# Optimization experiments

Measured on AMD Instinct MI355X. Metric: run time of the kernel, lower is better.

## Reference

```python
import jax, jax.numpy as jnp
import numpy as np

N = 100_000   # nodes
E = 1_600_000 # edges (avg degree 16)
D = 128       # dim == dim_out
NEG_SLOPE = 0.2  # PyG GATConv default


def setup_inputs() -> dict:
    key = jax.random.key(0)
    ks = jax.random.split(key, 11)
    s = 1.0 / np.sqrt(D)
    return {
        "x": jax.random.normal(ks[0], (N, D), jnp.float32),
        "edge_index": jax.random.randint(ks[1], (2, E), 0, N, jnp.int32),
        "W1": jax.random.normal(ks[2], (D, D), jnp.float32) * s,
        "a_src1": jax.random.normal(ks[3], (D,), jnp.float32) * s,
        "a_dst1": jax.random.normal(ks[4], (D,), jnp.float32) * s,
        "b1": jnp.zeros((D,), jnp.float32),
        "W2": jax.random.normal(ks[5], (D, D), jnp.float32) * s,
        "a_src2": jax.random.normal(ks[6], (D,), jnp.float32) * s,
        "a_dst2": jax.random.normal(ks[7], (D,), jnp.float32) * s,
        "b2": jnp.zeros((D,), jnp.float32),
    }


def gat_conv(x, W, a_src, a_dst, b, src, dst, n):
    # PyG GATConv, heads=1: message flows src (j) -> dst (i)
    h = x @ W                              # [n, d]
    al_src = h @ a_src                     # per-node src attention logit
    al_dst = h @ a_dst                     # per-node dst attention logit
    e = jax.nn.leaky_relu(al_src[src] + al_dst[dst], NEG_SLOPE)  # [E']
    # softmax over incoming edges of each destination node (segment softmax)
    m = jax.ops.segment_max(e, dst, num_segments=n)
    e = jnp.exp(e - m[dst])
    z = jax.ops.segment_sum(e, dst, num_segments=n)
    alpha = e / z[dst]                     # [E']
    out = jax.ops.segment_sum(h[src] * alpha[:, None], dst, num_segments=n)
    return out + b


def reference(x, edge_index, W1, a_src1, a_dst1, b1, W2, a_src2, a_dst2, b2):
    n = x.shape[0]
    loop = jnp.arange(n, dtype=edge_index.dtype)
    src = jnp.concatenate([edge_index[0], loop])  # add_self_loops=True
    dst = jnp.concatenate([edge_index[1], loop])
    h = gat_conv(x, W1, a_src1, a_dst1, b1, src, dst, n)
    # self_loops=True -> residual=False; dropout in eval mode = identity
    return gat_conv(h, W2, a_src2, a_dst2, b2, src, dst, n)
```

## Files before the change

### kernel.cpp

```cpp
#include <hip/hip_runtime.h>
#include <hip/hip_bf16.h>
#include <math.h>

#define D 128
#define LRELU_SLOPE 0.2f
#define BSH 9
#define BSZ 512
#define BCAP 10240
#define SC_CHUNK 2048

typedef __attribute__((ext_vector_type(8))) short bf16x8;
typedef __attribute__((ext_vector_type(4))) float f32x4;

__device__ __forceinline__ float lrelu(float x){ return x > 0.f ? x : LRELU_SLOPE * x; }

__device__ __forceinline__ unsigned short bf16_rn(float x){
  unsigned int u = __float_as_uint(x);
  return (unsigned short)((u + 0x7FFFu + ((u >> 16) & 1u)) >> 16);
}
__device__ __forceinline__ float bf16_lo_f(unsigned int u){ return __uint_as_float(u << 16); }
__device__ __forceinline__ float bf16_hi_f(unsigned int u){ return __uint_as_float(u & 0xFFFF0000u); }

__device__ __forceinline__ unsigned int enc_f(float f){
  unsigned int u = __float_as_uint(f);
  return (u & 0x80000000u) ? ~u : (u | 0x80000000u);
}
__device__ __forceinline__ float dec_f(unsigned int e){
  return __uint_as_float((e & 0x80000000u) ? (e & 0x7FFFFFFFu) : ~e);
}

__device__ __forceinline__ int colmap(int p){ return ((p & 7) << 4) + (p >> 3); }

__global__ __launch_bounds__(256) void prep_kernel(const float* __restrict__ W1,
    const float* __restrict__ W2,
    const float* __restrict__ as1, const float* __restrict__ ad1,
    const float* __restrict__ as2, const float* __restrict__ ad2,
    const float* __restrict__ b1,
    unsigned short* __restrict__ Whf1, unsigned short* __restrict__ Wlf1,
    unsigned short* __restrict__ Whf2, unsigned short* __restrict__ Wlf2,
    unsigned short* __restrict__ Whfx1, unsigned short* __restrict__ Wlfx1,
    unsigned short* __restrict__ Whfx2, unsigned short* __restrict__ Wlfx2,
    float* __restrict__ bias_perm1,
    unsigned int* __restrict__ mx, int* __restrict__ bcur, int nbuck)
{
  __shared__ float wa[2][128];
  int blk = blockIdx.x;
  if (blk < 128){
    bool layer2 = (blk >= 64);
    const float* W = layer2 ? W2 : W1;
    unsigned short* Whf = layer2 ? Whf2 : Whf1;
    unsigned short* Wlf = layer2 ? Wlf2 : Wlf1;
    int t = (blk & 63)*256 + threadIdx.x;
    int k  = t >> 7;
    int nn = t & 127;
    float w = W[t];
    unsigned short h = bf16_rn(w);
    float whf = __uint_as_float(((unsigned int)h) << 16);
    unsigned short l = bf16_rn(w - whf);
    int ks = layer2 ? (((k & 15) << 3) + (k >> 4)) : k;
    int kc = ks >> 5, l4 = (ks >> 3) & 3, e = ks & 7;
    int cf = nn >> 4, l15 = nn & 15;
    int idx = ((kc*8 + cf)*64 + l4*16 + l15)*8 + e;
    Whf[idx] = h; Wlf[idx] = l;
    return;
  }
  int layer = blk - 128;
  const float* W  = layer ? W2 : W1;
  const float* as = layer ? as2 : as1;
  const float* ad = layer ? ad2 : ad1;
  unsigned short* Whfx = layer ? Whfx2 : Whfx1;
  unsigned short* Wlfx = layer ? Wlfx2 : Wlfx1;
  int t = threadIdx.x;
  if (t < 2) mx[layer*2 + t] = 0u;
  if (layer == 0 && t < nbuck) bcur[t] = t * BCAP;
  if (layer == 0 && t < 128) bias_perm1[t] = b1[colmap(t)];

  int row = t & 127;
  const float* a = (t >> 7) ? ad : as;
  float s = 0.f;
  #pragma unroll 8
  for (int c = 0; c < 128; c += 4){
    float4 wv = *(const float4*)&W[row*128 + c];
    s += wv.x*a[c] + wv.y*a[c+1] + wv.z*a[c+2] + wv.w*a[c+3];
  }
  wa[t >> 7][row] = s;
  __syncthreads();

  int kc = t >> 6, lane = t & 63;
  int l15 = lane & 15, l4 = lane >> 4;
  unsigned short hh[8], ll[8];
  #pragma unroll
  for (int e = 0; e < 8; ++e){
    int ks = (kc*4 + l4)*8 + e;
    int k  = layer ? colmap(ks) : ks;
    float v = (l15 == 0) ? wa[0][k] : ((l15 == 1) ? wa[1][k] : 0.f);
    unsigned short h = bf16_rn(v);
    hh[e] = h;
    ll[e] = bf16_rn(v - __uint_as_float(((unsigned)h) << 16));
  }
  #pragma unroll
  for (int e = 0; e < 8; ++e){ Whfx[t*8 + e] = hh[e]; Wlfx[t*8 + e] = ll[e]; }
}

__global__ __launch_bounds__(256) void bucket_csr_kernel(const unsigned int* __restrict__ ebuf,
    const int* __restrict__ bcur, int2* __restrict__ rowrange, int* __restrict__ colb,
    int n, int nbuck){
  __shared__ int c[512];
  __shared__ int ps[256];
  int b = blockIdx.x;
  int t = threadIdx.x;
  int base = b * BCAP;
  int end  = bcur[b];
  c[t] = 0; c[t+256] = 0;
  __syncthreads();
  for (int i = base + t; i < end; i += 256)
    atomicAdd(&c[ebuf[i] & (BSZ-1)], 1);
  __syncthreads();
  int a0 = c[2*t], a1 = c[2*t+1];
  int pair = a0 + a1;
  ps[t] = pair;
  __syncthreads();
  #pragma unroll
  for (int d = 1; d < 256; d <<= 1){
    int add = (t >= d) ? ps[t-d] : 0;
    __syncthreads();
    ps[t] += add;
    __syncthreads();
  }
  int excl = ps[t] - pair;
  __syncthreads();
  int lo = b << BSH;
  int g0 = lo + 2*t, g1 = g0 + 1;
  if (g0 < n) rowrange[g0] = make_int2(base + excl,      base + excl + a0);
  if (g1 < n) rowrange[g1] = make_int2(base + excl + a0, base + excl + a0 + a1);
  c[2*t]   = excl;
  c[2*t+1] = excl + a0;
  __syncthreads();
  for (int i = base + t; i < end; i += 256){
    unsigned int p = ebuf[i];
    int dlo = p & (BSZ-1);
    int pos = base + atomicAdd(&c[dlo], 1);
    colb[pos] = (int)(p >> BSH);
  }
}

__global__ __launch_bounds__(256) void gemm1_scatter_kernel(const float* __restrict__ X,
    const unsigned short* __restrict__ Whf, const unsigned short* __restrict__ Wlf,
    const unsigned short* __restrict__ Whfx, const unsigned short* __restrict__ Wlfx,
    unsigned short* __restrict__ Hb, float* __restrict__ ALs, float* __restrict__ ALd,
    unsigned int* __restrict__ mx, int n, int sc_blocks,
    const int* __restrict__ src, const int* __restrict__ dst, int E,
    int* __restrict__ bcur, unsigned int* __restrict__ ebuf, int nbuck)
{
  __shared__ unsigned short Xh[128*128];
  __shared__ float redS[4], redD[4];
  int tid  = threadIdx.x;

  if (blockIdx.x < sc_blocks){
    int* h  = (int*)Xh;
    int* cb = h + 256;
    int base = blockIdx.x * SC_CHUNK;
    int end = base + SC_CHUNK; if (end > E) end = E;
    h[tid] = 0;
    __syncthreads();
    for (int e = base + tid; e < end; e += 256)
      atomicAdd(&h[dst[e] >> BSH], 1);
    __syncthreads();
    if (tid < nbuck){
      cb[tid] = h[tid] ? atomicAdd(&bcur[tid], h[tid]) : 0;
      h[tid] = 0;
    }
    __syncthreads();
    for (int e = base + tid; e < end; e += 256){
      int d = dst[e];
      int b = d >> BSH;
      int lpos = atomicAdd(&h[b], 1);
      ebuf[cb[b] + lpos] = ((unsigned int)src[e] << BSH) | (unsigned int)(d & (BSZ-1));
    }
    return;
  }

  int lane = tid & 63;
  int wave = tid >> 6;
  int row0 = (blockIdx.x - sc_blocks) * 128;
  int c4   = tid & 31;

  #pragma unroll
  for (int half = 0; half < 2; ++half){
    float4 v[8];
    #pragma unroll
    for (int i = 0; i < 8; ++i){
      int it = half*8 + i;
      int f  = it*256 + tid;
      int r  = f >> 5;
      int gr = row0 + r;
      v[i] = make_float4(0.f,0.f,0.f,0.f);
      if (gr < n) v[i] = ((const float4*)(X + (size_t)gr*D))[c4];
    }
    #pragma unroll
    for (int i = 0; i < 8; ++i){
      int it = half*8 + i;
      int f  = it*256 + tid;
      int r  = f >> 5;
      unsigned short h0 = bf16_rn(v[i].x);
      unsigned short h1 = bf16_rn(v[i].y);
      unsigned short h2 = bf16_rn(v[i].z);
      unsigned short h3 = bf16_rn(v[i].w);
      int g   = (c4 >> 1) ^ (r & 7);
      int idx = r*128 + (g << 3) + ((c4 & 1) << 2);
      *(uint2*)&Xh[idx] = make_uint2((unsigned)h0 | ((unsigned)h1<<16),
                                     (unsigned)h2 | ((unsigned)h3<<16));
    }
  }
  __syncthreads();

  int l15 = lane & 15;
  int l4  = lane >> 4;

  f32x4 acc[2][8];
  f32x4 acc2[2];
  #pragma unroll
  for (int rf = 0; rf < 2; ++rf){
    #pragma unroll
    for (int cf = 0; cf < 8; ++cf)
      acc[rf][cf] = (f32x4){0.f, 0.f, 0.f, 0.f};
    acc2[rf] = (f32x4){0.f, 0.f, 0.f, 0.f};
  }

  #pragma unroll
  for (int kc = 0; kc < 4; ++kc){
    int g = kc*4 + l4;
    bf16x8 ah[2];
    #pragma unroll
    for (int rf = 0; rf < 2; ++rf){
      int r   = wave*32 + rf*16 + l15;
      int idx = r*128 + ((g ^ (r & 7)) << 3);
      ah[rf] = *(const bf16x8*)&Xh[idx];
    }
    #pragma unroll
    for (int cf = 0; cf < 8; ++cf){
      int foff = ((kc*8 + cf) << 9) + (lane << 3);
      bf16x8 bh = *(const bf16x8*)&Whf[foff];
      bf16x8 bl = *(const bf16x8*)&Wlf[foff];
      #pragma unroll
      for (int rf = 0; rf < 2; ++rf){
        acc[rf][cf] = __builtin_amdgcn_mfma_f32_16x16x32_bf16(ah[rf], bh, acc[rf][cf], 0, 0, 0);
        acc[rf][cf] = __builtin_amdgcn_mfma_f32_16x16x32_bf16(ah[rf], bl, acc[rf][cf], 0, 0, 0);
      }
    }
    {
      int foffx = ((kc << 6) + lane) << 3;
      bf16x8 bhx = *(const bf16x8*)&Whfx[foffx];
      bf16x8 blx = *(const bf16x8*)&Wlfx[foffx];
      #pragma unroll
      for (int rf = 0; rf < 2; ++rf){
        acc2[rf] = __builtin_amdgcn_mfma_f32_16x16x32_bf16(ah[rf], bhx, acc2[rf], 0, 0, 0);
        acc2[rf] = __builtin_amdgcn_mfma_f32_16x16x32_bf16(ah[rf], blx, acc2[rf], 0, 0, 0);
      }
    }
  }

  float ms = -3e38f, md = -3e38f;
  #pragma unroll
  for (int rf = 0; rf < 2; ++rf){
    #pragma unroll
    for (int reg = 0; reg < 4; ++reg){
      int gr = row0 + wave*32 + rf*16 + l4*4 + reg;
      if (gr < n){
        unsigned int p0 = (unsigned)bf16_rn(acc[rf][0][reg]) | ((unsigned)bf16_rn(acc[rf][1][reg]) << 16);
        unsigned int p1 = (unsigned)bf16_rn(acc[rf][2][reg]) | ((unsigned)bf16_rn(acc[rf][3][reg]) << 16);
        unsigned int p2 = (unsigned)bf16_rn(acc[rf][4][reg]) | ((unsigned)bf16_rn(acc[rf][5][reg]) << 16);
        unsigned int p3 = (unsigned)bf16_rn(acc[rf][6][reg]) | ((unsigned)bf16_rn(acc[rf][7][reg]) << 16);
        ((uint4*)(Hb + (size_t)gr*D))[l15] = make_uint4(p0, p1, p2, p3);
        if (l15 == 0){      ALs[gr] = acc2[rf][reg]; ms = fmaxf(ms, acc2[rf][reg]); }
        else if (l15 == 1){ ALd[gr] = acc2[rf][reg]; md = fmaxf(md, acc2[rf][reg]); }
      }
    }
  }
  #pragma unroll
  for (int off = 32; off >= 1; off >>= 1){
    ms = fmaxf(ms, __shfl_xor(ms, off));
    md = fmaxf(md, __shfl_xor(md, off));
  }
  if (lane == 0){ redS[wave] = ms; redD[wave] = md; }
  __syncthreads();
  if (tid == 0){
    float a = fmaxf(fmaxf(redS[0], redS[1]), fmaxf(redS[2], redS[3]));
    float b = fmaxf(fmaxf(redD[0], redD[1]), fmaxf(redD[2], redD[3]));
    atomicMax(&mx[0], enc_f(a));
    atomicMax(&mx[1], enc_f(b));
  }
}

__global__ __launch_bounds__(256) void gemm2_kernel(const unsigned short* __restrict__ Xb,
    const unsigned short* __restrict__ Whf, const unsigned short* __restrict__ Wlf,
    const unsigned short* __restrict__ Whfx, const unsigned short* __restrict__ Wlfx,
    unsigned short* __restrict__ Hb, float* __restrict__ ALs, float* __restrict__ ALd,
    unsigned int* __restrict__ mx, int n)
{
  __shared__ unsigned short Xh[128*128];
  __shared__ float redS[4], redD[4];
  int tid  = threadIdx.x;
  int lane = tid & 63;
  int wave = tid >> 6;
  int row0 = blockIdx.x * 128;

  const uint4* X4 = (const uint4*)Xb;
  {
    uint4 v[8];
    #pragma unroll
    for (int it = 0; it < 8; ++it){
      int f  = it*256 + tid;
      int r  = f >> 4;
      int pg = f & 15;
      int gr = row0 + r;
      v[it] = make_uint4(0u,0u,0u,0u);
      if (gr < n) v[it] = X4[(size_t)gr*16 + pg];
    }
    #pragma unroll
    for (int it = 0; it < 8; ++it){
      int f  = it*256 + tid;
      int r  = f >> 4;
      int pg = f & 15;
      *(uint4*)&Xh[r*128 + ((pg ^ (r & 7)) << 3)] = v[it];
    }
  }
  __syncthreads();

  int l15 = lane & 15;
  int l4  = lane >> 4;

  f32x4 acc[2][8];
  f32x4 acc2[2];
  #pragma unroll
  for (int rf = 0; rf < 2; ++rf){
    #pragma unroll
    for (int cf = 0; cf < 8; ++cf)
      acc[rf][cf] = (f32x4){0.f, 0.f, 0.f, 0.f};
    acc2[rf] = (f32x4){0.f, 0.f, 0.f, 0.f};
  }

  #pragma unroll
  for (int kc = 0; kc < 4; ++kc){
    int g = kc*4 + l4;
    bf16x8 ah[2];
    #pragma unroll
    for (int rf = 0; rf < 2; ++rf){
      int r   = wave*32 + rf*16 + l15;
      int idx = r*128 + ((g ^ (r & 7)) << 3);
      ah[rf] = *(const bf16x8*)&Xh[idx];
    }
    #pragma unroll
    for (int cf = 0; cf < 8; ++cf){
      int foff = ((kc*8 + cf) << 9) + (lane << 3);
      bf16x8 bh = *(const bf16x8*)&Whf[foff];
      bf16x8 bl = *(const bf16x8*)&Wlf[foff];
      #pragma unroll
      for (int rf = 0; rf < 2; ++rf){
        acc[rf][cf] = __builtin_amdgcn_mfma_f32_16x16x32_bf16(ah[rf], bh, acc[rf][cf], 0, 0, 0);
        acc[rf][cf] = __builtin_amdgcn_mfma_f32_16x16x32_bf16(ah[rf], bl, acc[rf][cf], 0, 0, 0);
      }
    }
    {
      int foffx = ((kc << 6) + lane) << 3;
      bf16x8 bhx = *(const bf16x8*)&Whfx[foffx];
      bf16x8 blx = *(const bf16x8*)&Wlfx[foffx];
      #pragma unroll
      for (int rf = 0; rf < 2; ++rf){
        acc2[rf] = __builtin_amdgcn_mfma_f32_16x16x32_bf16(ah[rf], bhx, acc2[rf], 0, 0, 0);
        acc2[rf] = __builtin_amdgcn_mfma_f32_16x16x32_bf16(ah[rf], blx, acc2[rf], 0, 0, 0);
      }
    }
  }

  float ms = -3e38f, md = -3e38f;
  #pragma unroll
  for (int rf = 0; rf < 2; ++rf){
    #pragma unroll
    for (int reg = 0; reg < 4; ++reg){
      int gr = row0 + wave*32 + rf*16 + l4*4 + reg;
      if (gr < n){
        unsigned int p0 = (unsigned)bf16_rn(acc[rf][0][reg]) | ((unsigned)bf16_rn(acc[rf][1][reg]) << 16);
        unsigned int p1 = (unsigned)bf16_rn(acc[rf][2][reg]) | ((unsigned)bf16_rn(acc[rf][3][reg]) << 16);
        unsigned int p2 = (unsigned)bf16_rn(acc[rf][4][reg]) | ((unsigned)bf16_rn(acc[rf][5][reg]) << 16);
        unsigned int p3 = (unsigned)bf16_rn(acc[rf][6][reg]) | ((unsigned)bf16_rn(acc[rf][7][reg]) << 16);
        ((uint4*)(Hb + (size_t)gr*D))[l15] = make_uint4(p0, p1, p2, p3);
        if (l15 == 0){      ALs[gr] = acc2[rf][reg]; ms = fmaxf(ms, acc2[rf][reg]); }
        else if (l15 == 1){ ALd[gr] = acc2[rf][reg]; md = fmaxf(md, acc2[rf][reg]); }
      }
    }
  }
  #pragma unroll
  for (int off = 32; off >= 1; off >>= 1){
    ms = fmaxf(ms, __shfl_xor(ms, off));
    md = fmaxf(md, __shfl_xor(md, off));
  }
  if (lane == 0){ redS[wave] = ms; redD[wave] = md; }
  __syncthreads();
  if (tid == 0){
    float a = fmaxf(fmaxf(redS[0], redS[1]), fmaxf(redS[2], redS[3]));
    float b = fmaxf(fmaxf(redD[0], redD[1]), fmaxf(redD[2], redD[3]));
    atomicMax(&mx[0], enc_f(a));
    atomicMax(&mx[1], enc_f(b));
  }
}

template<bool BF16OUT>
__global__ __launch_bounds__(256) void agg_kernel(const unsigned short* __restrict__ Hb,
    const float* __restrict__ ALs, const float* __restrict__ ALd,
    const unsigned int* __restrict__ mx,
    const int2* __restrict__ rowrange, const int* __restrict__ colb,
    const float* __restrict__ bias, void* __restrict__ outv, int n)
{
  __shared__ unsigned int sArr[256];
  __shared__ float wArr[256];
  int gtid = blockIdx.x*blockDim.x + threadIdx.x;
  int node = gtid >> 6;
  int lane = threadIdx.x & 63;
  int wbase = threadIdx.x & 192;
  if (node >= n) return;

  float M = lrelu(dec_f(mx[0]) + dec_f(mx[1]));

  int2 rr = rowrange[node];
  int beg = rr.x, end = rr.y;
  float ald = ALd[node];
  float ws = __expf(lrelu(ALs[node] + ald) - M);

  const unsigned int* H2 = (const unsigned int*)Hb;
  unsigned int us = H2[(unsigned)(node*64 + lane)];
  float2 acc; acc.x = ws * bf16_lo_f(us); acc.y = ws * bf16_hi_f(us);
  float zl = 0.f;

  for (int c = beg; c < end; c += 64){
    int j = c + lane;
    bool valid = j < end;
    int s_l = valid ? colb[j] : 0;
    float w_l = valid ? __expf(lrelu(ALs[s_l] + ald) - M) : 0.f;
    zl += w_l;

    sArr[threadIdx.x] = (unsigned)s_l;
    wArr[threadIdx.x] = w_l;

    int cnt = end - c; if (cnt > 64) cnt = 64;
    int q = 0;
    for (; q + 8 <= cnt; q += 8){
      unsigned int ss[8]; float ww[8]; unsigned int u[8];
      #pragma unroll
      for (int p = 0; p < 8; ++p){ ss[p] = sArr[wbase + q + p]; ww[p] = wArr[wbase + q + p]; }
      #pragma unroll
      for (int p = 0; p < 8; ++p) u[p] = H2[(unsigned)(ss[p]*64u + lane)];
      #pragma unroll
      for (int p = 0; p < 8; ++p){
        acc.x += ww[p]*bf16_lo_f(u[p]);
        acc.y += ww[p]*bf16_hi_f(u[p]);
      }
    }
    for (; q < cnt; ++q){
      unsigned int u = H2[(unsigned)(sArr[wbase + q]*64u + lane)];
      float w = wArr[wbase + q];
      acc.x += w*bf16_lo_f(u); acc.y += w*bf16_hi_f(u);
    }
  }

  #pragma unroll
  for (int off = 32; off >= 1; off >>= 1) zl += __shfl_xor(zl, off);
  float zi = 1.f / (zl + ws);
  acc.x *= zi; acc.y *= zi;

  if constexpr (BF16OUT){
    float2 bp = ((const float2*)bias)[lane];
    unsigned int w = (unsigned)bf16_rn(acc.x + bp.x) | ((unsigned)bf16_rn(acc.y + bp.y) << 16);
    ((unsigned int*)outv)[(unsigned)(node*64 + lane)] = w;
  } else {
    int q0 = (lane >> 4) + ((lane & 7) << 3);
    int q1 = q0 + 4;
    int hsel = (lane >> 3) & 1;
    float x0 = __shfl(acc.x, q0), y0 = __shfl(acc.y, q0);
    float x1 = __shfl(acc.x, q1), y1 = __shfl(acc.y, q1);
    float v0 = hsel ? y0 : x0;
    float v1 = hsel ? y1 : x1;
    float2 b2 = ((const float2*)bias)[lane];
    ((float2*)outv)[(size_t)node*64 + lane] = make_float2(v0 + b2.x, v1 + b2.y);
  }
}

extern "C" void kernel_launch(void* const* d_in, const int* in_sizes, int n_in,
                              void* d_out, int out_size, void* d_ws, size_t ws_size,
                              hipStream_t stream)
{
  const float* x   = (const float*)d_in[0];
  const int*   ei  = (const int*)  d_in[1];
  const float* W1  = (const float*)d_in[2];
  const float* as1 = (const float*)d_in[3];
  const float* ad1 = (const float*)d_in[4];
  const float* b1  = (const float*)d_in[5];
  const float* W2  = (const float*)d_in[6];
  const float* as2 = (const float*)d_in[7];
  const float* ad2 = (const float*)d_in[8];
  const float* b2  = (const float*)d_in[9];

  int n = in_sizes[0] / D;
  int E = in_sizes[1] / 2;
  const int* src = ei;
  const int* dst = ei + E;
  int nbuck = (n + BSZ - 1) >> BSH;

  char* base = (char*)d_ws;
  size_t off = 0;
  auto alloc = [&](size_t bytes) -> char* {
    char* p = base + off;
    off = (off + bytes + 255) & ~(size_t)255;
    return p;
  };
  unsigned short* hb  = (unsigned short*)alloc((size_t)n*D*2);
  unsigned short* hb2 = (unsigned short*)alloc((size_t)n*D*2);
  float* als    = (float*)alloc((size_t)n*4);
  float* ald    = (float*)alloc((size_t)n*4);
  int2* rowrange = (int2*)alloc((size_t)n*8);
  int* bcur     = (int*)alloc(256*4);
  unsigned int* mx = (unsigned int*)alloc(4*4);
  float* bias_perm1 = (float*)alloc(128*4);
  unsigned short* whf1 = (unsigned short*)alloc(16384*2);
  unsigned short* wlf1 = (unsigned short*)alloc(16384*2);
  unsigned short* whf2 = (unsigned short*)alloc(16384*2);
  unsigned short* wlf2 = (unsigned short*)alloc(16384*2);
  unsigned short* whfx1 = (unsigned short*)alloc(2048*2);
  unsigned short* wlfx1 = (unsigned short*)alloc(2048*2);
  unsigned short* whfx2 = (unsigned short*)alloc(2048*2);
  unsigned short* wlfx2 = (unsigned short*)alloc(2048*2);
  unsigned int* ebuf = (unsigned int*)alloc((size_t)nbuck*BCAP*4);
  int* colb = (int*)alloc((size_t)nbuck*BCAP*4);

  float* out = (float*)d_out;

  int sc_blocks = (E + SC_CHUNK - 1) / SC_CHUNK;
  int ntiles = (n + 127)/128;
  int aggblocks = (int)(((size_t)n*64 + 255)/256);

  prep_kernel<<<130, 256, 0, stream>>>(W1, W2, as1, ad1, as2, ad2, b1,
                                       whf1, wlf1, whf2, wlf2,
                                       whfx1, wlfx1, whfx2, wlfx2,
                                       bias_perm1, mx, bcur, nbuck);
  gemm1_scatter_kernel<<<sc_blocks + ntiles, 256, 0, stream>>>(
      x, whf1, wlf1, whfx1, wlfx1, hb, als, ald, mx, n, sc_blocks,
      src, dst, E, bcur, ebuf, nbuck);
  bucket_csr_kernel<<<nbuck, 256, 0, stream>>>(ebuf, bcur, rowrange, colb, n, nbuck);
  agg_kernel<true>  <<<aggblocks, 256, 0, stream>>>(hb, als, ald, mx,   rowrange, colb, bias_perm1, hb2, n);
  gemm2_kernel      <<<ntiles, 256, 0, stream>>>(hb2, whf2, wlf2, whfx2, wlfx2, hb, als, ald, mx+2, n);
  agg_kernel<false> <<<aggblocks, 256, 0, stream>>>(hb, als, ald, mx+2, rowrange, colb, b2, out, n);
}
```

Before: 256.8 us.

## Merge edge-bucket scatter into every GEMM1 block instead of separate scatter blocks

Removes the dedicated scatter blocks and instead has each GEMM1 tile block first bucket a contiguous chunk of edges (E divided by number of tiles) before doing its GEMM tile. Scatter histograms move to their own shared arrays rather than aliasing the GEMM tile buffer. The aim is to cut the grid size and balance scatter work across the same blocks that do the matmul. The tradeoff is that every block now serializes scatter then GEMM, and the extra shared memory could lower occupancy.

```diff
diff --git a/kernel.cpp b/kernel.cpp
--- a/kernel.cpp
+++ b/kernel.cpp
@@ -7,7 +7,6 @@
 #define BSH 9
 #define BSZ 512
 #define BCAP 10240
-#define SC_CHUNK 2048
 
 typedef __attribute__((ext_vector_type(8))) short bf16x8;
 typedef __attribute__((ext_vector_type(4))) float f32x4;
@@ -148,41 +147,42 @@
     const unsigned short* __restrict__ Whf, const unsigned short* __restrict__ Wlf,
     const unsigned short* __restrict__ Whfx, const unsigned short* __restrict__ Wlfx,
     unsigned short* __restrict__ Hb, float* __restrict__ ALs, float* __restrict__ ALd,
-    unsigned int* __restrict__ mx, int n, int sc_blocks,
+    unsigned int* __restrict__ mx, int n, int ec,
     const int* __restrict__ src, const int* __restrict__ dst, int E,
     int* __restrict__ bcur, unsigned int* __restrict__ ebuf, int nbuck)
 {
   __shared__ unsigned short Xh[128*128];
+  __shared__ int hs[256];
+  __shared__ int cbs[256];
   __shared__ float redS[4], redD[4];
   int tid  = threadIdx.x;
 
-  if (blockIdx.x < sc_blocks){
-    int* h  = (int*)Xh;
-    int* cb = h + 256;
-    int base = blockIdx.x * SC_CHUNK;
-    int end = base + SC_CHUNK; if (end > E) end = E;
-    h[tid] = 0;
-    __syncthreads();
-    for (int e = base + tid; e < end; e += 256)
-      atomicAdd(&h[dst[e] >> BSH], 1);
-    __syncthreads();
-    if (tid < nbuck){
-      cb[tid] = h[tid] ? atomicAdd(&bcur[tid], h[tid]) : 0;
-      h[tid] = 0;
-    }
-    __syncthreads();
-    for (int e = base + tid; e < end; e += 256){
-      int d = dst[e];
-      int b = d >> BSH;
-      int lpos = atomicAdd(&h[b], 1);
-      ebuf[cb[b] + lpos] = ((unsigned int)src[e] << BSH) | (unsigned int)(d & (BSZ-1));
-    }
-    return;
+  {
+    int base = blockIdx.x * ec;
+    int end = base + ec; if (end > E) end = E;
+    if (base < E){
+      hs[tid] = 0;
+      __syncthreads();
+      for (int e = base + tid; e < end; e += 256)
+        atomicAdd(&hs[dst[e] >> BSH], 1);
+      __syncthreads();
+      if (tid < nbuck){
+        cbs[tid] = hs[tid] ? atomicAdd(&bcur[tid], hs[tid]) : 0;
+        hs[tid] = 0;
+      }
+      __syncthreads();
+      for (int e = base + tid; e < end; e += 256){
+        int d = dst[e];
+        int b = d >> BSH;
+        int lpos = atomicAdd(&hs[b], 1);
+        ebuf[cbs[b] + lpos] = ((unsigned int)src[e] << BSH) | (unsigned int)(d & (BSZ-1));
+      }
+    }
   }
 
   int lane = tid & 63;
   int wave = tid >> 6;
-  int row0 = (blockIdx.x - sc_blocks) * 128;
+  int row0 = blockIdx.x * 128;
   int c4   = tid & 31;
 
   #pragma unroll
@@ -534,16 +534,16 @@
 
   float* out = (float*)d_out;
 
-  int sc_blocks = (E + SC_CHUNK - 1) / SC_CHUNK;
   int ntiles = (n + 127)/128;
+  int ec = (E + ntiles - 1)/ntiles;
   int aggblocks = (int)(((size_t)n*64 + 255)/256);
 
   prep_kernel<<<130, 256, 0, stream>>>(W1, W2, as1, ad1, as2, ad2, b1,
                                        whf1, wlf1, whf2, wlf2,
                                        whfx1, wlfx1, whfx2, wlfx2,
                                        bias_perm1, mx, bcur, nbuck);
-  gemm1_scatter_kernel<<<sc_blocks + ntiles, 256, 0, stream>>>(
-      x, whf1, wlf1, whfx1, wlfx1, hb, als, ald, mx, n, sc_blocks,
+  gemm1_scatter_kernel<<<ntiles, 256, 0, stream>>>(
+      x, whf1, wlf1, whfx1, wlfx1, hb, als, ald, mx, n, ec,
       src, dst, E, bcur, ebuf, nbuck);
   bucket_csr_kernel<<<nbuck, 256, 0, stream>>>(ebuf, bcur, rowrange, colb, n, nbuck);
   agg_kernel<true>  <<<aggblocks, 256, 0, stream>>>(hb, als, ald, mx,   rowrange, colb, bias_perm1, hb2, n);
```

Result: slower. 267.6 us (+4.2%).
